# Performance work log

Measured on AMD Instinct MI355X. Metric: run time of the kernel, lower is better.

The kernel has to match this reference:

```python
import jax, jax.numpy as jnp
import numpy as np

NUM_HEADS = 16  # matches init_kwargs
LN_EPS = 1e-5   # torch LayerNorm default

def setup_inputs() -> dict:
    key = jax.random.key(0)
    ks = jax.random.split(key, 8)
    N, L, D = 2, 2048, 1024
    DH = D // NUM_HEADS
    kt = 3
    s = lambda fan: 1.0 / np.sqrt(fan)
    return {
        "x": jax.random.normal(ks[0], (N, L, D), jnp.float32),
        "in_proj_w": jax.random.normal(ks[1], (3 * D, D), jnp.float32) * s(D),
        "in_proj_b": jax.random.normal(ks[2], (3 * D,), jnp.float32) * s(D),
        "conv_w": jax.random.normal(ks[3], (DH, kt), jnp.float32) * s(kt),
        "conv_b": jax.random.normal(ks[4], (DH,), jnp.float32) * s(kt),
        "ln_g": jnp.ones((DH,), jnp.float32),
        "ln_b": jnp.zeros((DH,), jnp.float32),
        "out_w": jax.random.normal(ks[5], (D, D), jnp.float32) * s(D),
        "out_b": jax.random.normal(ks[6], (D,), jnp.float32) * s(D),
    }

def _forward(x, in_proj_w, in_proj_b, conv_w, conv_b, ln_g, ln_b, out_w, out_b):
    N, L, D = x.shape
    H = NUM_HEADS
    DH = D // H
    kt = conv_w.shape[-1]
    scaling = DH ** -0.5

    qkv = x @ in_proj_w.T + in_proj_b                      # [N, L, 3D]
    q, k, v = jnp.split(qkv, 3, axis=-1)

    def heads(t):  # [N, L, D] -> [N*H, L, DH]
        return t.reshape(N, L, H, DH).transpose(0, 2, 1, 3).reshape(N * H, L, DH)

    qh, kh, vh = heads(q), heads(k), heads(v)              # [NH, L, DH]

    # causal depthwise conv1d over time on head_dim channels
    qt = qh.transpose(0, 2, 1)                             # [NH, DH, L]
    qp = jnp.pad(qt, ((0, 0), (0, 0), (kt - 1, 0)))        # left pad (causal)
    conv = conv_b[None, :, None]
    for j in range(kt):
        conv = conv + qp[:, :, j:j + L] * conv_w[None, :, j, None]
    g = jax.nn.gelu(conv, approximate=False)               # torch GELU (erf)
    g = g.transpose(0, 2, 1)                               # [NH, L, DH]

    mu = g.mean(-1, keepdims=True)
    var = ((g - mu) ** 2).mean(-1, keepdims=True)          # biased var (torch LN)
    ln = (g - mu) / jnp.sqrt(var + LN_EPS) * ln_g + ln_b

    q_rel = ln.mean(axis=1)                                # [NH, DH]
    Wk = jnp.einsum('nd,nld->nl', q_rel * scaling, kh)     # [NH, L]
    Wn = Wk / (jnp.abs(Wk).sum(axis=1, keepdims=True) + 1e-6)

    # causal convolution of V with per-head kernel Wn (lag-indexed Toeplitz GEMM)
    t_idx = jnp.arange(L)
    lag = t_idx[:, None] - t_idx[None, :]                  # [L, L], t - s
    T = jnp.where(lag >= 0, Wn[:, jnp.clip(lag, 0)], 0.0)  # [NH, L, L]
    attn = jnp.einsum('nts,nsd->ntd', T, vh)               # [NH, L, DH]

    merged = attn.reshape(N, H, L, DH).transpose(0, 2, 1, 3).reshape(N, L, D)
    output = merged @ out_w.T + out_b
    mock_attn_weights = jnp.ones((N, L), x.dtype) / L
    return output, mock_attn_weights

def reference(x, in_proj_w, in_proj_b, conv_w, conv_b, ln_g, ln_b, out_w, out_b):
    return _forward(x, in_proj_w, in_proj_b, conv_w, conv_b, ln_g, ln_b, out_w, out_b)
```

## Files before the change

### kernel.cpp

```cpp
#include <hip/hip_runtime.h>
#include <hip/hip_bf16.h>
#include <hip/hip_runtime_api.h>

#define NB 2
#define LL 2048
#define DD 1024
#define HH 16
#define DH 64
#define ROWS (NB*LL)

typedef short bf16x8 __attribute__((ext_vector_type(8)));
typedef float f32x4  __attribute__((ext_vector_type(4)));

__device__ inline float b2f(unsigned short u) {
    union { float f; unsigned int i; } c; c.i = ((unsigned int)u) << 16; return c.f;
}
__device__ inline unsigned short f2b(float f) {
    __hip_bfloat16 h = __float2bfloat16(f);
    union { __hip_bfloat16 h; unsigned short u; } c; c.h = h; return c.u;
}

__global__ __launch_bounds__(256) void fused_cast_init(const float* __restrict__ x,
                                                       const float* __restrict__ in_w,
                                                       const float* __restrict__ out_w,
                                                       __hip_bfloat16* __restrict__ xb,
                                                       __hip_bfloat16* __restrict__ wqb,
                                                       __hip_bfloat16* __restrict__ wvb,
                                                       __hip_bfloat16* __restrict__ owb,
                                                       float* __restrict__ q_rel,
                                                       float* __restrict__ absacc)
{
    const long idx = (long)blockIdx.x * 256 + threadIdx.x;
    const float4* src;
    __hip_bfloat16* dst;
    long off;
    if (idx < 1048576)      { src = (const float4*)x;     dst = xb;  off = idx; }
    else if (idx < 1310720) { src = (const float4*)in_w;  dst = wqb; off = idx - 1048576; }
    else if (idx < 1572864) { src = (const float4*)(in_w + (size_t)2 * DD * DD);
                              dst = wvb; off = idx - 1310720; }
    else                    { src = (const float4*)out_w; dst = owb; off = idx - 1572864; }

    const float4 v = src[off];
    union { short4 s; __hip_bfloat16 h[4]; } u;
    u.h[0] = __float2bfloat16(v.x);
    u.h[1] = __float2bfloat16(v.y);
    u.h[2] = __float2bfloat16(v.z);
    u.h[3] = __float2bfloat16(v.w);
    ((short4*)dst)[off] = u.s;

    if (blockIdx.x == 0) {
        for (int j = threadIdx.x; j < 32 * DH; j += 256) q_rel[j] = 0.f;
        if (threadIdx.x < 32) absacc[threadIdx.x] = 0.f;
    }
}

template <typename TC>
__global__ __launch_bounds__(256) void gemm_bt_lds(const __hip_bfloat16* __restrict__ A,
                                                   const __hip_bfloat16* __restrict__ Bm,
                                                   const float* __restrict__ bias,
                                                   TC* __restrict__ C,
                                                   float* __restrict__ mock,
                                                   int M, int N, int K)
{
    __shared__ short As[128 * 32];
    __shared__ short Bs[128 * 32];

    const int tid  = threadIdx.x;
    const int lane = tid & 63;
    const int w    = tid >> 6;
    const int wm   = w >> 1;
    const int wn   = w & 1;
    const int l15  = lane & 15;
    const int quad = lane >> 4;

    const int n0 = blockIdx.x * 128;
    const int m0 = blockIdx.y * 128;

    const int lr  = lane >> 2;
    const int lsg = lane & 3;

    const __hip_bfloat16* gA0 = A  + (size_t)(m0 + w * 32 + lr) * K + lsg * 8;
    const __hip_bfloat16* gB0 = Bm + (size_t)(n0 + w * 32 + lr) * K + lsg * 8;
    short* lA0 = As + (w * 32) * 32;
    short* lA1 = As + (w * 32 + 16) * 32;
    short* lB0 = Bs + (w * 32) * 32;
    short* lB1 = Bs + (w * 32 + 16) * 32;

    f32x4 acc[4][4];
    #pragma unroll
    for (int i = 0; i < 4; ++i)
        #pragma unroll
        for (int j = 0; j < 4; ++j) acc[i][j] = {0.f, 0.f, 0.f, 0.f};

    for (int k0 = 0; k0 < K; k0 += 32) {
        __syncthreads();
        __builtin_amdgcn_global_load_lds((const void*)(gA0 + k0),                  (void*)lA0, 16, 0, 0);
        __builtin_amdgcn_global_load_lds((const void*)(gA0 + (size_t)16 * K + k0), (void*)lA1, 16, 0, 0);
        __builtin_amdgcn_global_load_lds((const void*)(gB0 + k0),                  (void*)lB0, 16, 0, 0);
        __builtin_amdgcn_global_load_lds((const void*)(gB0 + (size_t)16 * K + k0), (void*)lB1, 16, 0, 0);
        __syncthreads();

        bf16x8 af[4], bf[4];
        #pragma unroll
        for (int mt = 0; mt < 4; ++mt)
            af[mt] = *(const bf16x8*)(As + (wm * 64 + mt * 16 + l15) * 32 + quad * 8);
        #pragma unroll
        for (int nt = 0; nt < 4; ++nt)
            bf[nt] = *(const bf16x8*)(Bs + (wn * 64 + nt * 16 + l15) * 32 + quad * 8);

        #pragma unroll
        for (int mt = 0; mt < 4; ++mt)
            #pragma unroll
            for (int nt = 0; nt < 4; ++nt)
                acc[mt][nt] = __builtin_amdgcn_mfma_f32_16x16x32_bf16(
                    af[mt], bf[nt], acc[mt][nt], 0, 0, 0);
    }

    #pragma unroll
    for (int nt = 0; nt < 4; ++nt) {
        const int col = n0 + wn * 64 + nt * 16 + l15;
        const float bv = bias[col];
        #pragma unroll
        for (int mt = 0; mt < 4; ++mt) {
            #pragma unroll
            for (int r = 0; r < 4; ++r) {
                const int row = m0 + wm * 64 + mt * 16 + quad * 4 + r;
                float v = acc[mt][nt][r] + bv;
                v = isfinite(v) ? v : 0.f;
                if constexpr (sizeof(TC) == 2)
                    C[(size_t)row * N + col] = __float2bfloat16(v);
                else
                    C[(size_t)row * N + col] = v;
            }
        }
    }

    if (mock != nullptr && blockIdx.x == 0 && blockIdx.y == 0) {
        for (int i = tid; i < NB * LL; i += 256) mock[i] = 1.0f / (float)LL;
    }
}

__global__ __launch_bounds__(256) void gemm_vT_lds(const __hip_bfloat16* __restrict__ A,
                                                   const __hip_bfloat16* __restrict__ Bm,
                                                   const float* __restrict__ bias,
                                                   __hip_bfloat16* __restrict__ vT,
                                                   int M, int N, int K)
{
    __shared__ short As[128 * 32];
    __shared__ short Bs[128 * 32];

    const int tid  = threadIdx.x;
    const int lane = tid & 63;
    const int w    = tid >> 6;
    const int wm   = w >> 1;
    const int wn   = w & 1;
    const int l15  = lane & 15;
    const int quad = lane >> 4;

    const int n0 = blockIdx.x * 128;
    const int m0 = blockIdx.y * 128;

    const int lr  = lane >> 2;
    const int lsg = lane & 3;

    const __hip_bfloat16* gA0 = A  + (size_t)(m0 + w * 32 + lr) * K + lsg * 8;
    const __hip_bfloat16* gB0 = Bm + (size_t)(n0 + w * 32 + lr) * K + lsg * 8;
    short* lA0 = As + (w * 32) * 32;
    short* lA1 = As + (w * 32 + 16) * 32;
    short* lB0 = Bs + (w * 32) * 32;
    short* lB1 = Bs + (w * 32 + 16) * 32;

    f32x4 acc[4][4];
    #pragma unroll
    for (int i = 0; i < 4; ++i)
        #pragma unroll
        for (int j = 0; j < 4; ++j) acc[i][j] = {0.f, 0.f, 0.f, 0.f};

    for (int k0 = 0; k0 < K; k0 += 32) {
        __syncthreads();
        __builtin_amdgcn_global_load_lds((const void*)(gA0 + k0),                  (void*)lA0, 16, 0, 0);
        __builtin_amdgcn_global_load_lds((const void*)(gA0 + (size_t)16 * K + k0), (void*)lA1, 16, 0, 0);
        __builtin_amdgcn_global_load_lds((const void*)(gB0 + k0),                  (void*)lB0, 16, 0, 0);
        __builtin_amdgcn_global_load_lds((const void*)(gB0 + (size_t)16 * K + k0), (void*)lB1, 16, 0, 0);
        __syncthreads();

        bf16x8 af[4], bf[4];
        #pragma unroll
        for (int mt = 0; mt < 4; ++mt)
            af[mt] = *(const bf16x8*)(As + (wm * 64 + mt * 16 + l15) * 32 + quad * 8);
        #pragma unroll
        for (int nt = 0; nt < 4; ++nt)
            bf[nt] = *(const bf16x8*)(Bs + (wn * 64 + nt * 16 + l15) * 32 + quad * 8);

        #pragma unroll
        for (int mt = 0; mt < 4; ++mt)
            #pragma unroll
            for (int nt = 0; nt < 4; ++nt)
                acc[mt][nt] = __builtin_amdgcn_mfma_f32_16x16x32_bf16(
                    af[mt], bf[nt], acc[mt][nt], 0, 0, 0);
    }

    #pragma unroll
    for (int nt = 0; nt < 4; ++nt) {
        const int col = n0 + wn * 64 + nt * 16 + l15;
        const float bv = bias[col];
        #pragma unroll
        for (int mt = 0; mt < 4; ++mt) {
            const int row0 = m0 + wm * 64 + mt * 16 + quad * 4;
            const int nn = row0 >> 11;
            const int l  = row0 & (LL - 1);
            ushort4 u;
            float v0 = acc[mt][nt][0] + bv; v0 = isfinite(v0) ? v0 : 0.f;
            float v1 = acc[mt][nt][1] + bv; v1 = isfinite(v1) ? v1 : 0.f;
            float v2 = acc[mt][nt][2] + bv; v2 = isfinite(v2) ? v2 : 0.f;
            float v3 = acc[mt][nt][3] + bv; v3 = isfinite(v3) ? v3 : 0.f;
            u.x = f2b(v0); u.y = f2b(v1); u.z = f2b(v2); u.w = f2b(v3);
            *(ushort4*)(vT + ((size_t)(nn * 1024 + col)) * LL + l) = u;
        }
    }
}

__global__ __launch_bounds__(256) void conv_gelu_ln_part(const __hip_bfloat16* __restrict__ q,
                                                          const float* __restrict__ conv_w,
                                                          const float* __restrict__ conv_b,
                                                          const float* __restrict__ ln_g,
                                                          const float* __restrict__ ln_b,
                                                          float* __restrict__ q_rel)
{
    const int bx = blockIdx.x;
    const int nh = bx >> 4;
    const int lc = bx & 15;
    const int n  = nh >> 4;
    const int h  = nh & 15;
    const int tid = threadIdx.x;
    const int d   = tid & 63;
    const int wv  = tid >> 6;
    const int l0  = lc * 128;

    __shared__ unsigned short qs[130 * 64];
    __shared__ float red[4 * 64];

    for (int idx = tid; idx < 130 * 8; idx += 256) {
        const int r   = idx >> 3;
        const int seg = idx & 7;
        const int l   = l0 - 2 + r;
        uint4 val = {0u, 0u, 0u, 0u};
        if (l >= 0)
            val = *(const uint4*)(q + (size_t)(n * LL + l) * DD + h * DH + seg * 8);
        *(uint4*)(qs + r * 64 + seg * 8) = val;
    }
    __syncthreads();

    const float w0 = conv_w[d * 3 + 0];
    const float w1 = conv_w[d * 3 + 1];
    const float w2 = conv_w[d * 3 + 2];
    const float cb = conv_b[d];
    const float lg = ln_g[d];
    const float lb = ln_b[d];

    float part = 0.f;
    for (int i = 0; i < 32; ++i) {
        const int r = wv * 32 + i + 2;
        const float xm2 = b2f(qs[(r - 2) * 64 + d]);
        const float xm1 = b2f(qs[(r - 1) * 64 + d]);
        const float x0  = b2f(qs[r * 64 + d]);
        const float c   = cb + w0 * xm2 + w1 * xm1 + w2 * x0;
        const float g   = 0.5f * c * (1.f + erff(c * 0.70710678118654752f));

        float s = g;
        #pragma unroll
        for (int off = 32; off > 0; off >>= 1) s += __shfl_xor(s, off);
        const float mu = s * (1.f / 64.f);

        const float dg = g - mu;
        float s2 = dg * dg;
        #pragma unroll
        for (int off = 32; off > 0; off >>= 1) s2 += __shfl_xor(s2, off);
        const float var = s2 * (1.f / 64.f);

        part += dg * rsqrtf(var + 1e-5f) * lg + lb;
    }

    red[wv * 64 + d] = part;
    __syncthreads();
    if (tid < 64) {
        const float t = red[d] + red[64 + d] + red[128 + d] + red[192 + d];
        atomicAdd(&q_rel[nh * DH + d], t * (0.125f / (float)LL));
    }
}

__global__ __launch_bounds__(256) void proj_p2(const float* __restrict__ in_w,
                                               const float* __restrict__ in_b,
                                               const float* __restrict__ q_rel,
                                               __hip_bfloat16* __restrict__ pb,
                                               float* __restrict__ beta)
{
    const int bx = blockIdx.x;
    const int nh = bx >> 2;
    const int cc = bx & 3;
    const int h  = nh & 15;
    const int tid = threadIdx.x;

    __shared__ float qs[64];
    if (tid < 64) qs[tid] = q_rel[nh * DH + tid];
    __syncthreads();

    const float* W = in_w + ((size_t)DD + h * DH) * DD;
    const int c = cc * 256 + tid;
    float a = 0.f;
    #pragma unroll 8
    for (int d = 0; d < 64; ++d)
        a += qs[d] * W[(size_t)d * DD + c];
    pb[(size_t)nh * DD + c] = __float2bfloat16(a);

    if (cc == 0 && tid < 64) {
        float b = qs[tid] * in_b[DD + h * DH + tid];
        #pragma unroll
        for (int off = 32; off > 0; off >>= 1) b += __shfl_xor(b, off);
        if (tid == 0) beta[nh] = b;
    }
}

__global__ __launch_bounds__(256) void wk_mfma(const __hip_bfloat16* __restrict__ xb,
                                               const __hip_bfloat16* __restrict__ pb,
                                               const float* __restrict__ beta,
                                               float* __restrict__ WnRaw,
                                               float* __restrict__ absacc)
{
    __shared__ short As[128 * 32];
    __shared__ short Bs[16 * 32];

    const int bx   = blockIdx.x;
    const int n    = bx >> 4;
    const int lt   = bx & 15;
    const int tid  = threadIdx.x;
    const int lane = tid & 63;
    const int w    = tid >> 6;
    const int l15  = lane & 15;
    const int quad = lane >> 4;
    const int m0   = lt * 128;

    const int lr  = lane >> 2;
    const int lsg = lane & 3;

    const __hip_bfloat16* gA0 = xb + (size_t)(n * LL + m0 + w * 32 + lr) * DD + lsg * 8;
    const __hip_bfloat16* gB0 = pb + (size_t)(n * 16 + lr) * DD + lsg * 8;
    short* lA0 = As + (w * 32) * 32;
    short* lA1 = As + (w * 32 + 16) * 32;

    f32x4 acc0 = {0.f,0.f,0.f,0.f};
    f32x4 acc1 = {0.f,0.f,0.f,0.f};

    for (int k0 = 0; k0 < DD; k0 += 32) {
        __syncthreads();
        __builtin_amdgcn_global_load_lds((const void*)(gA0 + k0),                   (void*)lA0, 16, 0, 0);
        __builtin_amdgcn_global_load_lds((const void*)(gA0 + (size_t)16 * DD + k0), (void*)lA1, 16, 0, 0);
        if (w == 0)
            __builtin_amdgcn_global_load_lds((const void*)(gB0 + k0), (void*)Bs, 16, 0, 0);
        __syncthreads();

        bf16x8 a0 = *(const bf16x8*)(As + (w * 32 + l15) * 32 + quad * 8);
        bf16x8 a1 = *(const bf16x8*)(As + (w * 32 + 16 + l15) * 32 + quad * 8);
        bf16x8 b  = *(const bf16x8*)(Bs + l15 * 32 + quad * 8);

        acc0 = __builtin_amdgcn_mfma_f32_16x16x32_bf16(a0, b, acc0, 0, 0, 0);
        acc1 = __builtin_amdgcn_mfma_f32_16x16x32_bf16(a1, b, acc1, 0, 0, 0);
    }

    const int hd = n * 16 + l15;
    const float bet = beta[hd];
    float asum = 0.f;
    f32x4 accs[2] = {acc0, acc1};
    #pragma unroll
    for (int mt = 0; mt < 2; ++mt) {
        #pragma unroll
        for (int r = 0; r < 4; ++r) {
            const int l = m0 + w * 32 + mt * 16 + quad * 4 + r;
            float v = accs[mt][r] + bet;
            v = isfinite(v) ? v : 0.f;
            WnRaw[(size_t)hd * LL + l] = v;
            asum += fabsf(v);
        }
    }
    asum += __shfl_xor(asum, 16);
    asum += __shfl_xor(asum, 32);
    if (quad == 0) atomicAdd(&absacc[hd], asum);
}

__global__ __launch_bounds__(256) void toeplitz2(const __hip_bfloat16* __restrict__ vT,
                                                 const float* __restrict__ WnRaw,
                                                 const float* __restrict__ absacc,
                                                 __hip_bfloat16* __restrict__ merged)
{
    const int bx = blockIdx.x;
    const int tt = 31 - (bx >> 5);
    const int nh = bx & 31;
    const int n  = nh >> 4;
    const int h  = nh & 15;
    const int tid  = threadIdx.x;
    const int lane = tid & 63;
    const int w    = tid >> 6;
    const int l15  = lane & 15;
    const int quad = lane >> 4;
    const int t0   = tt * 64;

    __shared__ unsigned short wfull[2112];
    __shared__ unsigned short vbuf[2][64 * 64];

    const float inv = 1.f / (absacc[nh] + 1e-6f);
    const float* wnr = WnRaw + (size_t)nh * LL;
    const __hip_bfloat16* vtb = vT + (size_t)nh * 64 * LL;

    const int wlim = t0 + 127;
    for (int i = tid; i < wlim; i += 256) {
        const int lag = i - 63;
        wfull[i] = f2b(lag >= 0 ? wnr[lag] * inv : 0.f);
    }

    const int srow = lane >> 3;
    const int sseg = ((lane & 7) + srow) & 7;

    #pragma unroll
    for (int j = 0; j < 2; ++j) {
        const int r0 = w * 16 + j * 8;
        __builtin_amdgcn_global_load_lds(
            (const void*)(vtb + (size_t)(r0 + srow) * LL + sseg * 8),
            (void*)(&vbuf[0][r0 * 64]), 16, 0, 0);
    }

    f32x4 acc0 = {0.f,0.f,0.f,0.f};
    f32x4 acc1 = {0.f,0.f,0.f,0.f};
    f32x4 acc2 = {0.f,0.f,0.f,0.f};
    f32x4 acc3 = {0.f,0.f,0.f,0.f};

    int cur = 0;
    __syncthreads();
    for (int st = 0; st <= tt; ++st) {
        if (st < tt) {
            const int s0n = (st + 1) * 64;
            #pragma unroll
            for (int j = 0; j < 2; ++j) {
                const int r0 = w * 16 + j * 8;
                __builtin_amdgcn_global_load_lds(
                    (const void*)(vtb + (size_t)(r0 + srow) * LL + s0n + sseg * 8),
                    (void*)(&vbuf[cur ^ 1][r0 * 64]), 16, 0, 0);
            }
        }
        const int delta = t0 - st * 64;
        const unsigned short* vb = vbuf[cur];

        #pragma unroll
        for (int c = 0; c < 2; ++c) {
            union { bf16x8 v8; unsigned short u[8]; } af;
            const int I0 = 63 + delta + (w * 16 + l15) - c * 32 - quad * 8;
            #pragma unroll
            for (int j = 0; j < 8; ++j) af.u[j] = wfull[I0 - j];

            const int seg = c * 4 + quad;
            const int co  = ((seg - l15) & 7) * 8;
            bf16x8 bf0 = *(const bf16x8*)(vb + (0  + l15) * 64 + co);
            bf16x8 bf1 = *(const bf16x8*)(vb + (16 + l15) * 64 + co);
            bf16x8 bf2 = *(const bf16x8*)(vb + (32 + l15) * 64 + co);
            bf16x8 bf3 = *(const bf16x8*)(vb + (48 + l15) * 64 + co);

            acc0 = __builtin_amdgcn_mfma_f32_16x16x32_bf16(af.v8, bf0, acc0, 0, 0, 0);
            acc1 = __builtin_amdgcn_mfma_f32_16x16x32_bf16(af.v8, bf1, acc1, 0, 0, 0);
            acc2 = __builtin_amdgcn_mfma_f32_16x16x32_bf16(af.v8, bf2, acc2, 0, 0, 0);
            acc3 = __builtin_amdgcn_mfma_f32_16x16x32_bf16(af.v8, bf3, acc3, 0, 0, 0);
        }
        __syncthreads();
        cur ^= 1;
    }

    f32x4 accs[4] = {acc0, acc1, acc2, acc3};
    #pragma unroll
    for (int ct = 0; ct < 4; ++ct) {
        const int col = ct * 16 + l15;
        #pragma unroll
        for (int r = 0; r < 4; ++r) {
            const int t = t0 + w * 16 + quad * 4 + r;
            merged[(size_t)(n * LL + t) * DD + h * DH + col] = __float2bfloat16(accs[ct][r]);
        }
    }
}

extern "C" void kernel_launch(void* const* d_in, const int* in_sizes, int n_in,
                              void* d_out, int out_size, void* d_ws, size_t ws_size,
                              hipStream_t stream)
{
    const float* x      = (const float*)d_in[0];
    const float* in_w   = (const float*)d_in[1];
    const float* in_b   = (const float*)d_in[2];
    const float* conv_w = (const float*)d_in[3];
    const float* conv_b = (const float*)d_in[4];
    const float* ln_g   = (const float*)d_in[5];
    const float* ln_b   = (const float*)d_in[6];
    const float* out_w  = (const float*)d_in[7];
    const float* out_b  = (const float*)d_in[8];

    __hip_bfloat16* xb    = (__hip_bfloat16*)d_ws;
    __hip_bfloat16* wqb   = xb + (size_t)ROWS * DD;
    __hip_bfloat16* wvb   = wqb + (size_t)DD * DD;
    __hip_bfloat16* owb   = wvb + (size_t)DD * DD;
    float*          WnRaw = (float*)(owb + (size_t)DD * DD);
    float*          q_rel = WnRaw + 32 * LL;
    __hip_bfloat16* pb    = (__hip_bfloat16*)(q_rel + 32 * DH);
    float*          beta  = (float*)(pb + 32 * DD);

    __hip_bfloat16* qbuf   = (__hip_bfloat16*)d_out;
    __hip_bfloat16* vTbuf  = (__hip_bfloat16*)d_out + (size_t)ROWS * DD;
    __hip_bfloat16* merged = xb;
    float*          out    = (float*)d_out;
    float*          out2   = out + (size_t)ROWS * DD;
    float*          absacc = out2;

    fused_cast_init<<<7168, 256, 0, stream>>>(x, in_w, out_w, xb, wqb, wvb, owb,
                                              q_rel, absacc);

    gemm_bt_lds<__hip_bfloat16><<<dim3(DD / 128, ROWS / 128), 256, 0, stream>>>(
        xb, wqb, in_b, qbuf, nullptr, ROWS, DD, DD);

    conv_gelu_ln_part<<<512, 256, 0, stream>>>(qbuf, conv_w, conv_b, ln_g, ln_b, q_rel);

    proj_p2<<<128, 256, 0, stream>>>(in_w, in_b, q_rel, pb, beta);

    wk_mfma<<<32, 256, 0, stream>>>(xb, pb, beta, WnRaw, absacc);

    gemm_vT_lds<<<dim3(DD / 128, ROWS / 128), 256, 0, stream>>>(
        xb, wvb, in_b + 2 * DD, vTbuf, ROWS, DD, DD);

    toeplitz2<<<32 * 32, 256, 0, stream>>>(vTbuf, WnRaw, absacc, merged);

    gemm_bt_lds<float><<<dim3(DD / 128, ROWS / 128), 256, 0, stream>>>(
        merged, owb, out_b, out, out2, ROWS, DD, DD);
}
```

Measured before the change: 245.0 us.

## Fuse Q/V projection GEMMs, double-tile Toeplitz blocks, narrow output GEMM tiles

Q and V projections now run as one GEMM launch over the adjacent bf16 Q and V weight rows. Each output column is routed either to the row-major Q buffer or to the transposed V buffer, and the launch moves ahead of the Wk computation. The Toeplitz kernel now has each block compute two 64-row time tiles that share every staged V chunk, which halves the V reloads but doubles accumulator registers and still leaves uneven block workloads. The output projection uses 128x64 tiles to double the block count for occupancy, at the cost of less A-tile reuse per block.

Result: faster. 216.4 us (-11.6%).

```diff
diff --git a/kernel.cpp b/kernel.cpp
--- a/kernel.cpp
+++ b/kernel.cpp
@@ -54,13 +54,11 @@
     }
 }
 
-template <typename TC>
-__global__ __launch_bounds__(256) void gemm_bt_lds(const __hip_bfloat16* __restrict__ A,
-                                                   const __hip_bfloat16* __restrict__ Bm,
-                                                   const float* __restrict__ bias,
-                                                   TC* __restrict__ C,
-                                                   float* __restrict__ mock,
-                                                   int M, int N, int K)
+__global__ __launch_bounds__(256) void gemm_qv(const __hip_bfloat16* __restrict__ A,
+                                               const __hip_bfloat16* __restrict__ Bm,
+                                               const float* __restrict__ in_b,
+                                               __hip_bfloat16* __restrict__ q,
+                                               __hip_bfloat16* __restrict__ vT)
 {
     __shared__ short As[128 * 32];
     __shared__ short Bs[128 * 32];
@@ -75,6 +73,7 @@
 
     const int n0 = blockIdx.x * 128;
     const int m0 = blockIdx.y * 128;
+    const int K  = DD;
 
     const int lr  = lane >> 2;
     const int lsg = lane & 3;
@@ -118,61 +117,69 @@
 
     #pragma unroll
     for (int nt = 0; nt < 4; ++nt) {
-        const int col = n0 + wn * 64 + nt * 16 + l15;
-        const float bv = bias[col];
-        #pragma unroll
-        for (int mt = 0; mt < 4; ++mt) {
-            #pragma unroll
-            for (int r = 0; r < 4; ++r) {
-                const int row = m0 + wm * 64 + mt * 16 + quad * 4 + r;
-                float v = acc[mt][nt][r] + bv;
-                v = isfinite(v) ? v : 0.f;
-                if constexpr (sizeof(TC) == 2)
-                    C[(size_t)row * N + col] = __float2bfloat16(v);
-                else
-                    C[(size_t)row * N + col] = v;
+        const int colg = n0 + wn * 64 + nt * 16 + l15;
+        const float bv = (colg < DD) ? in_b[colg] : in_b[DD + colg];
+        if (colg < DD) {
+            #pragma unroll
+            for (int mt = 0; mt < 4; ++mt) {
+                #pragma unroll
+                for (int r = 0; r < 4; ++r) {
+                    const int row = m0 + wm * 64 + mt * 16 + quad * 4 + r;
+                    float v = acc[mt][nt][r] + bv;
+                    v = isfinite(v) ? v : 0.f;
+                    q[(size_t)row * DD + colg] = __float2bfloat16(v);
+                }
+            }
+        } else {
+            const int col = colg - DD;
+            #pragma unroll
+            for (int mt = 0; mt < 4; ++mt) {
+                const int row0 = m0 + wm * 64 + mt * 16 + quad * 4;
+                const int nn = row0 >> 11;
+                const int l  = row0 & (LL - 1);
+                ushort4 u;
+                float v0 = acc[mt][nt][0] + bv; v0 = isfinite(v0) ? v0 : 0.f;
+                float v1 = acc[mt][nt][1] + bv; v1 = isfinite(v1) ? v1 : 0.f;
+                float v2 = acc[mt][nt][2] + bv; v2 = isfinite(v2) ? v2 : 0.f;
+                float v3 = acc[mt][nt][3] + bv; v3 = isfinite(v3) ? v3 : 0.f;
+                u.x = f2b(v0); u.y = f2b(v1); u.z = f2b(v2); u.w = f2b(v3);
+                *(ushort4*)(vT + ((size_t)(nn * 1024 + col)) * LL + l) = u;
             }
         }
     }
-
-    if (mock != nullptr && blockIdx.x == 0 && blockIdx.y == 0) {
-        for (int i = tid; i < NB * LL; i += 256) mock[i] = 1.0f / (float)LL;
-    }
-}
-
-__global__ __launch_bounds__(256) void gemm_vT_lds(const __hip_bfloat16* __restrict__ A,
-                                                   const __hip_bfloat16* __restrict__ Bm,
-                                                   const float* __restrict__ bias,
-                                                   __hip_bfloat16* __restrict__ vT,
-                                                   int M, int N, int K)
+}
+
+__global__ __launch_bounds__(256) void gemm_out64(const __hip_bfloat16* __restrict__ A,
+                                                  const __hip_bfloat16* __restrict__ Bm,
+                                                  const float* __restrict__ bias,
+                                                  float* __restrict__ C,
+                                                  float* __restrict__ mock)
 {
     __shared__ short As[128 * 32];
-    __shared__ short Bs[128 * 32];
+    __shared__ short Bs[64 * 32];
 
     const int tid  = threadIdx.x;
     const int lane = tid & 63;
     const int w    = tid >> 6;
-    const int wm   = w >> 1;
-    const int wn   = w & 1;
     const int l15  = lane & 15;
     const int quad = lane >> 4;
 
-    const int n0 = blockIdx.x * 128;
+    const int n0 = blockIdx.x * 64;
     const int m0 = blockIdx.y * 128;
+    const int K  = DD;
 
     const int lr  = lane >> 2;
     const int lsg = lane & 3;
 
     const __hip_bfloat16* gA0 = A  + (size_t)(m0 + w * 32 + lr) * K + lsg * 8;
-    const __hip_bfloat16* gB0 = Bm + (size_t)(n0 + w * 32 + lr) * K + lsg * 8;
+    const __hip_bfloat16* gB0 = Bm + (size_t)(n0 + w * 16 + lr) * K + lsg * 8;
     short* lA0 = As + (w * 32) * 32;
     short* lA1 = As + (w * 32 + 16) * 32;
-    short* lB0 = Bs + (w * 32) * 32;
-    short* lB1 = Bs + (w * 32 + 16) * 32;
-
-    f32x4 acc[4][4];
-    #pragma unroll
-    for (int i = 0; i < 4; ++i)
+    short* lB0 = Bs + (w * 16) * 32;
+
+    f32x4 acc[2][4];
+    #pragma unroll
+    for (int i = 0; i < 2; ++i)
         #pragma unroll
         for (int j = 0; j < 4; ++j) acc[i][j] = {0.f, 0.f, 0.f, 0.f};
 
@@ -181,19 +188,18 @@
         __builtin_amdgcn_global_load_lds((const void*)(gA0 + k0),                  (void*)lA0, 16, 0, 0);
         __builtin_amdgcn_global_load_lds((const void*)(gA0 + (size_t)16 * K + k0), (void*)lA1, 16, 0, 0);
         __builtin_amdgcn_global_load_lds((const void*)(gB0 + k0),                  (void*)lB0, 16, 0, 0);
-        __builtin_amdgcn_global_load_lds((const void*)(gB0 + (size_t)16 * K + k0), (void*)lB1, 16, 0, 0);
-        __syncthreads();
-
-        bf16x8 af[4], bf[4];
-        #pragma unroll
-        for (int mt = 0; mt < 4; ++mt)
-            af[mt] = *(const bf16x8*)(As + (wm * 64 + mt * 16 + l15) * 32 + quad * 8);
+        __syncthreads();
+
+        bf16x8 af[2], bf[4];
+        #pragma unroll
+        for (int mt = 0; mt < 2; ++mt)
+            af[mt] = *(const bf16x8*)(As + (w * 32 + mt * 16 + l15) * 32 + quad * 8);
         #pragma unroll
         for (int nt = 0; nt < 4; ++nt)
-            bf[nt] = *(const bf16x8*)(Bs + (wn * 64 + nt * 16 + l15) * 32 + quad * 8);
-
-        #pragma unroll
-        for (int mt = 0; mt < 4; ++mt)
+            bf[nt] = *(const bf16x8*)(Bs + (nt * 16 + l15) * 32 + quad * 8);
+
+        #pragma unroll
+        for (int mt = 0; mt < 2; ++mt)
             #pragma unroll
             for (int nt = 0; nt < 4; ++nt)
                 acc[mt][nt] = __builtin_amdgcn_mfma_f32_16x16x32_bf16(
@@ -202,21 +208,22 @@
 
     #pragma unroll
     for (int nt = 0; nt < 4; ++nt) {
-        const int col = n0 + wn * 64 + nt * 16 + l15;
+        const int col = n0 + nt * 16 + l15;
         const float bv = bias[col];
         #pragma unroll
-        for (int mt = 0; mt < 4; ++mt) {
-            const int row0 = m0 + wm * 64 + mt * 16 + quad * 4;
-            const int nn = row0 >> 11;
-            const int l  = row0 & (LL - 1);
-            ushort4 u;
-            float v0 = acc[mt][nt][0] + bv; v0 = isfinite(v0) ? v0 : 0.f;
-            float v1 = acc[mt][nt][1] + bv; v1 = isfinite(v1) ? v1 : 0.f;
-            float v2 = acc[mt][nt][2] + bv; v2 = isfinite(v2) ? v2 : 0.f;
-            float v3 = acc[mt][nt][3] + bv; v3 = isfinite(v3) ? v3 : 0.f;
-            u.x = f2b(v0); u.y = f2b(v1); u.z = f2b(v2); u.w = f2b(v3);
-            *(ushort4*)(vT + ((size_t)(nn * 1024 + col)) * LL + l) = u;
+        for (int mt = 0; mt < 2; ++mt) {
+            #pragma unroll
+            for (int r = 0; r < 4; ++r) {
+                const int row = m0 + w * 32 + mt * 16 + quad * 4 + r;
+                float v = acc[mt][nt][r] + bv;
+                v = isfinite(v) ? v : 0.f;
+                C[(size_t)row * DD + col] = v;
+            }
         }
+    }
+
+    if (mock != nullptr && blockIdx.x == 0 && blockIdx.y == 0) {
+        for (int i = tid; i < NB * LL; i += 256) mock[i] = 1.0f / (float)LL;
     }
 }
 
@@ -387,13 +394,13 @@
     if (quad == 0) atomicAdd(&absacc[hd], asum);
 }
 
-__global__ __launch_bounds__(256) void toeplitz2(const __hip_bfloat16* __restrict__ vT,
-                                                 const float* __restrict__ WnRaw,
-                                                 const float* __restrict__ absacc,
-                                                 __hip_bfloat16* __restrict__ merged)
+__global__ __launch_bounds__(256) void toeplitz2p(const __hip_bfloat16* __restrict__ vT,
+                                                  const float* __restrict__ WnRaw,
+                                                  const float* __restrict__ absacc,
+                                                  __hip_bfloat16* __restrict__ merged)
 {
     const int bx = blockIdx.x;
-    const int tt = 31 - (bx >> 5);
+    const int a  = 15 - (bx >> 5);
     const int nh = bx & 31;
     const int n  = nh >> 4;
     const int h  = nh & 15;
@@ -402,18 +409,19 @@
     const int w    = tid >> 6;
     const int l15  = lane & 15;
     const int quad = lane >> 4;
-    const int t0   = tt * 64;
-
-    __shared__ unsigned short wfull[2112];
+    const int t0b  = a * 128;
+    const int tthi = 2 * a + 1;
+
+    __shared__ unsigned short wfull[2176];
     __shared__ unsigned short vbuf[2][64 * 64];
 
     const float inv = 1.f / (absacc[nh] + 1e-6f);
     const float* wnr = WnRaw + (size_t)nh * LL;
     const __hip_bfloat16* vtb = vT + (size_t)nh * 64 * LL;
 
-    const int wlim = t0 + 127;
+    const int wlim = t0b + 255;
     for (int i = tid; i < wlim; i += 256) {
-        const int lag = i - 63;
+        const int lag = i - 127;
         wfull[i] = f2b(lag >= 0 ? wnr[lag] * inv : 0.f);
     }
 
@@ -428,15 +436,14 @@
             (void*)(&vbuf[0][r0 * 64]), 16, 0, 0);
     }
 
-    f32x4 acc0 = {0.f,0.f,0.f,0.f};
-    f32x4 acc1 = {0.f,0.f,0.f,0.f};
-    f32x4 acc2 = {0.f,0.f,0.f,0.f};
-    f32x4 acc3 = {0.f,0.f,0.f,0.f};
+    f32x4 accL[4], accU[4];
+    #pragma unroll
+    for (int i = 0; i < 4; ++i) { accL[i] = {0.f,0.f,0.f,0.f}; accU[i] = {0.f,0.f,0.f,0.f}; }
 
     int cur = 0;
     __syncthreads();
-    for (int st = 0; st <= tt; ++st) {
-        if (st < tt) {
+    for (int st = 0; st <= tthi; ++st) {
+        if (st < tthi) {
             const int s0n = (st + 1) * 64;
             #pragma unroll
             for (int j = 0; j < 2; ++j) {
@@ -446,15 +453,17 @@
                     (void*)(&vbuf[cur ^ 1][r0 * 64]), 16, 0, 0);
             }
         }
-        const int delta = t0 - st * 64;
+        const int dL = t0b - st * 64;
         const unsigned short* vb = vbuf[cur];
 
         #pragma unroll
         for (int c = 0; c < 2; ++c) {
-            union { bf16x8 v8; unsigned short u[8]; } af;
-            const int I0 = 63 + delta + (w * 16 + l15) - c * 32 - quad * 8;
-            #pragma unroll
-            for (int j = 0; j < 8; ++j) af.u[j] = wfull[I0 - j];
+            union { bf16x8 v8; unsigned short u[8]; } afL, afU;
+            const int base = 127 + (w * 16 + l15) - c * 32 - quad * 8;
+            const int IL = base + dL;
+            const int IU = IL + 64;
+            #pragma unroll
+            for (int j = 0; j < 8; ++j) { afL.u[j] = wfull[IL - j]; afU.u[j] = wfull[IU - j]; }
 
             const int seg = c * 4 + quad;
             const int co  = ((seg - l15) & 7) * 8;
@@ -463,23 +472,27 @@
             bf16x8 bf2 = *(const bf16x8*)(vb + (32 + l15) * 64 + co);
             bf16x8 bf3 = *(const bf16x8*)(vb + (48 + l15) * 64 + co);
 
-            acc0 = __builtin_amdgcn_mfma_f32_16x16x32_bf16(af.v8, bf0, acc0, 0, 0, 0);
-            acc1 = __builtin_amdgcn_mfma_f32_16x16x32_bf16(af.v8, bf1, acc1, 0, 0, 0);
-            acc2 = __builtin_amdgcn_mfma_f32_16x16x32_bf16(af.v8, bf2, acc2, 0, 0, 0);
-            acc3 = __builtin_amdgcn_mfma_f32_16x16x32_bf16(af.v8, bf3, acc3, 0, 0, 0);
+            accL[0] = __builtin_amdgcn_mfma_f32_16x16x32_bf16(afL.v8, bf0, accL[0], 0, 0, 0);
+            accL[1] = __builtin_amdgcn_mfma_f32_16x16x32_bf16(afL.v8, bf1, accL[1], 0, 0, 0);
+            accL[2] = __builtin_amdgcn_mfma_f32_16x16x32_bf16(afL.v8, bf2, accL[2], 0, 0, 0);
+            accL[3] = __builtin_amdgcn_mfma_f32_16x16x32_bf16(afL.v8, bf3, accL[3], 0, 0, 0);
+            accU[0] = __builtin_amdgcn_mfma_f32_16x16x32_bf16(afU.v8, bf0, accU[0], 0, 0, 0);
+            accU[1] = __builtin_amdgcn_mfma_f32_16x16x32_bf16(afU.v8, bf1, accU[1], 0, 0, 0);
+            accU[2] = __builtin_amdgcn_mfma_f32_16x16x32_bf16(afU.v8, bf2, accU[2], 0, 0, 0);
+            accU[3] = __builtin_amdgcn_mfma_f32_16x16x32_bf16(afU.v8, bf3, accU[3], 0, 0, 0);
         }
         __syncthreads();
         cur ^= 1;
     }
 
-    f32x4 accs[4] = {acc0, acc1, acc2, acc3};
     #pragma unroll
     for (int ct = 0; ct < 4; ++ct) {
         const int col = ct * 16 + l15;
         #pragma unroll
         for (int r = 0; r < 4; ++r) {
-            const int t = t0 + w * 16 + quad * 4 + r;
-            merged[(size_t)(n * LL + t) * DD + h * DH + col] = __float2bfloat16(accs[ct][r]);
+            const int tL = t0b + w * 16 + quad * 4 + r;
+            merged[(size_t)(n * LL + tL) * DD + h * DH + col] = __float2bfloat16(accL[ct][r]);
+            merged[(size_t)(n * LL + tL + 64) * DD + h * DH + col] = __float2bfloat16(accU[ct][r]);
         }
     }
 }
@@ -517,8 +530,8 @@
     fused_cast_init<<<7168, 256, 0, stream>>>(x, in_w, out_w, xb, wqb, wvb, owb,
                                               q_rel, absacc);
 
-    gemm_bt_lds<__hip_bfloat16><<<dim3(DD / 128, ROWS / 128), 256, 0, stream>>>(
-        xb, wqb, in_b, qbuf, nullptr, ROWS, DD, DD);
+    gemm_qv<<<dim3(2048 / 128, ROWS / 128), 256, 0, stream>>>(
+        xb, wqb, in_b, qbuf, vTbuf);
 
     conv_gelu_ln_part<<<512, 256, 0, stream>>>(qbuf, conv_w, conv_b, ln_g, ln_b, q_rel);
 
@@ -526,11 +539,8 @@
 
     wk_mfma<<<32, 256, 0, stream>>>(xb, pb, beta, WnRaw, absacc);
 
-    gemm_vT_lds<<<dim3(DD / 128, ROWS / 128), 256, 0, stream>>>(
-        xb, wvb, in_b + 2 * DD, vTbuf, ROWS, DD, DD);
-
-    toeplitz2<<<32 * 32, 256, 0, stream>>>(vTbuf, WnRaw, absacc, merged);
-
-    gemm_bt_lds<float><<<dim3(DD / 128, ROWS / 128), 256, 0, stream>>>(
-        merged, owb, out_b, out, out2, ROWS, DD, DD);
-}
+    toeplitz2p<<<512, 256, 0, stream>>>(vTbuf, WnRaw, absacc, merged);
+
+    gemm_out64<<<dim3(DD / 64, ROWS / 128), 256, 0, stream>>>(
+        merged, owb, out_b, out, out2);
+}
```
